# Kernel tuning notes

Hardware: AMD Instinct MI355X
Metric: run time of the kernel (lower is better)

Reference implementation:

```python
import jax, jax.numpy as jnp
import numpy as np

N = 50000
E = 800000


def _degrees(src, dst):
    ones = jnp.ones((E,), dtype=jnp.float32)
    indeg = jax.ops.segment_sum(ones, dst, num_segments=N)
    outdeg = jax.ops.segment_sum(ones, src, num_segments=N)
    return indeg, outdeg


def _aggregate(h, src, dst):
    # update_all(copy_src, sum): gather src features, scatter-add to dst
    return jax.ops.segment_sum(h[src], dst, num_segments=N)


def _graph_conv(h, src, dst, innorm, outnorm, W, b):
    h = h * outnorm[:, None]
    h = _aggregate(h, src, dst)
    h = h * innorm[:, None]
    return h @ W + b


def setup_inputs() -> dict:
    key = jax.random.key(0)
    ks = jax.random.split(key, 8)
    d_in, d_hid, d_out = 128, 128, 64
    inp = {
        "features": jax.random.normal(ks[0], (N, d_in), dtype=jnp.float32),
        "src": jax.random.randint(ks[1], (E,), 0, N, dtype=jnp.int32),
        "dst": jax.random.randint(ks[2], (E,), 0, N, dtype=jnp.int32),
        "W0": jax.random.normal(ks[3], (d_in, d_hid), dtype=jnp.float32) / np.sqrt(d_in),
        "b0": jnp.zeros((d_hid,), dtype=jnp.float32),
        "W1": jax.random.normal(ks[4], (d_hid, d_hid), dtype=jnp.float32) / np.sqrt(d_hid),
        "b1": jnp.zeros((d_hid,), dtype=jnp.float32),
        "W2": jax.random.normal(ks[5], (d_hid, d_hid), dtype=jnp.float32) / np.sqrt(d_hid),
        "b2": jnp.zeros((d_hid,), dtype=jnp.float32),
        "W3": jax.random.normal(ks[6], (d_hid, d_out), dtype=jnp.float32) / np.sqrt(d_hid),
        "b3": jnp.zeros((d_out,), dtype=jnp.float32),
    }
    return inp


def reference(features, src, dst, W0, b0, W1, b1, W2, b2, W3, b3):
    indeg, outdeg = _degrees(src, dst)
    innorm = jnp.power(jnp.clip(indeg, 1.0, None), -0.5)
    outnorm = jnp.power(jnp.clip(outdeg, 1.0, None), -0.5)

    # input GraphConv + relu
    h = jax.nn.relu(_graph_conv(features, src, dst, innorm, outnorm, W0, b0))

    # GResConv blocks: graph_res=True, raw_res=True, dropout=0 (identity)
    for (W, b) in ((W1, b1), (W2, b2)):
        res = features * innorm[:, None]          # pre-norm (in-degree)
        res = _aggregate(res, src, dst)
        res = res * innorm[:, None]               # post-norm (in-degree)
        h = jax.nn.relu(_graph_conv(h, src, dst, innorm, outnorm, W, b) + res)

    # output GraphConv (no activation)
    return _graph_conv(h, src, dst, innorm, outnorm, W3, b3)
```

## Files before the change

kernel.cpp:

```cpp
#include <hip/hip_runtime.h>


#define GN 50000
#define GE 800000
#define SCAN_CHUNK 1024
#define DEG_BLOCKS 64
#define DEG_SLICE 12500
#define HALF_NODES 25000
#define HALF_WORDS 12500

typedef __attribute__((ext_vector_type(8))) short bf16x8;
typedef __attribute__((ext_vector_type(4))) float f32x4;

__device__ __forceinline__ float u2f(unsigned int u) { return __uint_as_float(u); }

__device__ __forceinline__ unsigned int bfr(float a) {
  unsigned int u = __float_as_uint(a);
  return (u + 0x7fffu + ((u >> 16) & 1u)) >> 16;
}
__device__ __forceinline__ unsigned int bfpack(float a, float b) {
  return bfr(a) | (bfr(b) << 16);
}
__device__ __forceinline__ void bfunpack8(uint4 u, float* f) {
  f[0] = u2f(u.x << 16); f[1] = u2f(u.x & 0xffff0000u);
  f[2] = u2f(u.y << 16); f[3] = u2f(u.y & 0xffff0000u);
  f[4] = u2f(u.z << 16); f[5] = u2f(u.z & 0xffff0000u);
  f[6] = u2f(u.w << 16); f[7] = u2f(u.w & 0xffff0000u);
}

__global__ __launch_bounds__(256) void degrees_lds_kernel(
    const int* __restrict__ src, const int* __restrict__ dst,
    unsigned int* __restrict__ partials, int E) {
  __shared__ unsigned int hist[HALF_WORDS];
  for (int i = threadIdx.x; i < HALF_WORDS; i += 256) hist[i] = 0u;
  __syncthreads();
  int b    = blockIdx.x & 63;
  int half = (blockIdx.x >> 6) & 1;
  int dir  = blockIdx.x >> 7;
  const int* __restrict__ idx = dir ? src : dst;
  int lo = half * HALF_NODES, hi = lo + HALF_NODES;
  int s = b * DEG_SLICE;
  int e = min(s + DEG_SLICE, E);
  for (int i = s + threadIdx.x; i < e; i += 256) {
    int node = idx[i];
    if (node >= lo && node < hi) {
      int local = node - lo;
      atomicAdd(&hist[local >> 1], 1u << ((local & 1) << 4));
    }
  }
  __syncthreads();
  unsigned int* outp = partials + (((size_t)dir * 2 + half) * DEG_BLOCKS + b) * HALF_WORDS;
  for (int i = threadIdx.x; i < HALF_WORDS; i += 256) outp[i] = hist[i];
}

__global__ void degrees_reduce_kernel(const unsigned int* __restrict__ partials,
                                      int* __restrict__ indeg, float* __restrict__ innorm,
                                      float* __restrict__ outnorm,
                                      unsigned int* __restrict__ rel16pk) {
  int g = blockIdx.x * blockDim.x + threadIdx.x;
  if (g >= 2 * HALF_WORDS) return;
  int half = (g >= HALF_WORDS) ? 1 : 0;
  int w = g - half * HALF_WORDS;
  int n0 = half * HALF_NODES + 2 * w;
  unsigned int inLo = 0, inHi = 0, outLo = 0, outHi = 0;
  const unsigned int* pIn  = partials + ((size_t)(0 * 2 + half) * DEG_BLOCKS) * HALF_WORDS + w;
  const unsigned int* pOut = partials + ((size_t)(1 * 2 + half) * DEG_BLOCKS) * HALF_WORDS + w;
#pragma unroll 4
  for (int b = 0; b < DEG_BLOCKS; b++) {
    rel16pk[((size_t)b * GN + n0) >> 1] = inLo | (inHi << 16);
    unsigned int v = pIn[(size_t)b * HALF_WORDS];
    inLo += v & 0xffffu; inHi += v >> 16;
    unsigned int u = pOut[(size_t)b * HALF_WORDS];
    outLo += u & 0xffffu; outHi += u >> 16;
  }
  indeg[n0]     = (int)inLo;
  indeg[n0 + 1] = (int)inHi;
  innorm[n0]      = rsqrtf((float)max((int)inLo, 1));
  innorm[n0 + 1]  = rsqrtf((float)max((int)inHi, 1));
  outnorm[n0]     = rsqrtf((float)max((int)outLo, 1));
  outnorm[n0 + 1] = rsqrtf((float)max((int)outHi, 1));
}

__global__ __launch_bounds__(256) void scan_blocksums(const int* __restrict__ deg,
                                                      int* __restrict__ bsums, int n) {
  int tid = threadIdx.x;
  int i = blockIdx.x * SCAN_CHUNK + tid * 4;
  int s = 0;
  if (i + 3 < n) {
    int4 v = *(const int4*)(deg + i);
    s = v.x + v.y + v.z + v.w;
  } else {
    for (int j = 0; j < 4; j++) if (i + j < n) s += deg[i + j];
  }
  for (int off = 32; off; off >>= 1) s += __shfl_down(s, off);
  __shared__ int ws[4];
  if ((tid & 63) == 0) ws[tid >> 6] = s;
  __syncthreads();
  if (tid == 0) bsums[blockIdx.x] = ws[0] + ws[1] + ws[2] + ws[3];
}

__global__ void scan_bsums(const int* __restrict__ bsums, int* __restrict__ bpref,
                           int nb, int* __restrict__ offsets, int n) {
  int tid = threadIdx.x;
  int v = (tid < nb) ? bsums[tid] : 0;
  int incl = v;
  for (int off = 1; off < 64; off <<= 1) {
    int t = __shfl_up(incl, off);
    if (tid >= off) incl += t;
  }
  if (tid < nb) bpref[tid] = incl - v;
  if (tid == 63) offsets[n] = incl;
}

__global__ __launch_bounds__(256) void scan_final(const int* __restrict__ deg,
                                                  const int* __restrict__ bpref,
                                                  int* __restrict__ offsets, int n) {
  int tid = threadIdx.x;
  int i = blockIdx.x * SCAN_CHUNK + tid * 4;
  int v[4];
#pragma unroll
  for (int j = 0; j < 4; j++) v[j] = (i + j < n) ? deg[i + j] : 0;
  int tsum = v[0] + v[1] + v[2] + v[3];
  int incl = tsum;
  for (int off = 1; off < 64; off <<= 1) {
    int t = __shfl_up(incl, off);
    if ((tid & 63) >= off) incl += t;
  }
  __shared__ int wsum[4];
  int wid = tid >> 6, lane = tid & 63;
  if (lane == 63) wsum[wid] = incl;
  __syncthreads();
  int wpref = 0;
  for (int w = 0; w < wid; w++) wpref += wsum[w];
  int run = bpref[blockIdx.x] + wpref + incl - tsum;
#pragma unroll
  for (int j = 0; j < 4; j++) {
    if (i + j < n) offsets[i + j] = run;
    run += v[j];
  }
}

__global__ __launch_bounds__(256) void fill_csr_lds_kernel(
    const int* __restrict__ src, const int* __restrict__ dst,
    const int* __restrict__ offsets, const unsigned short* __restrict__ rel16,
    int* __restrict__ csr, int E) {
  __shared__ unsigned int cnt[HALF_WORDS];
  for (int i = threadIdx.x; i < HALF_WORDS; i += 256) cnt[i] = 0u;
  __syncthreads();
  int b    = blockIdx.x & 63;
  int half = blockIdx.x >> 6;
  int lo = half * HALF_NODES, hi = lo + HALF_NODES;
  int s = b * DEG_SLICE;
  int e = min(s + DEG_SLICE, E);
  const unsigned short* relb = rel16 + (size_t)b * GN;
  for (int i = s + threadIdx.x; i < e; i += 256) {
    int d = dst[i];
    if (d >= lo && d < hi) {
      int local = d - lo;
      int sh = (local & 1) << 4;
      unsigned int old = atomicAdd(&cnt[local >> 1], 1u << sh);
      int rank = (int)((old >> sh) & 0xffffu);
      int pos = offsets[d] + (int)relb[d] + rank;
      csr[pos] = src[i];
    }
  }
}

__global__ __launch_bounds__(256) void f32_to_bf16_kernel(const float* __restrict__ in,
                                                          uint4* __restrict__ out, int n8) {
  int t = blockIdx.x * blockDim.x + threadIdx.x;
  if (t >= n8) return;
  const float4* in4 = (const float4*)in;
  float4 f0 = in4[2 * t], f1 = in4[2 * t + 1];
  uint4 o;
  o.x = bfpack(f0.x, f0.y); o.y = bfpack(f0.z, f0.w);
  o.z = bfpack(f1.x, f1.y); o.w = bfpack(f1.z, f1.w);
  out[t] = o;
}

__global__ __launch_bounds__(256) void wconvert_kernel(
    const float* __restrict__ W0, const float* __restrict__ W1,
    const float* __restrict__ W2, const float* __restrict__ W3,
    unsigned short* __restrict__ wt) {
  int e = blockIdx.x * 256 + threadIdx.x;
  if (e >= 3 * 16384 + 8192) return;
  int m, local, N;
  if (e < 49152) { m = e >> 14; local = e & 16383; N = 128; }
  else { m = 3; local = e - 49152; N = 64; }
  const float* W = (m == 0) ? W0 : (m == 1) ? W1 : (m == 2) ? W2 : W3;
  int k = local / N, n = local % N;
  float v = W[k * N + n];
  unsigned int hi = bfr(v);
  float rem = v - u2f(hi << 16);
  unsigned int lo = bfr(rem);
  size_t hibase = (m < 3) ? (size_t)m * 32768 : 98304;
  size_t lobase = hibase + ((m < 3) ? 16384 : 8192);
  wt[hibase + (size_t)n * 128 + k] = (unsigned short)hi;
  wt[lobase + (size_t)n * 128 + k] = (unsigned short)lo;
}

__global__ __launch_bounds__(256) void aggregate128_bf16_kernel(
    const uint4* __restrict__ hq, const float* __restrict__ gscale,
    const float* __restrict__ wscale, const int* __restrict__ offsets,
    const int* __restrict__ csr, uint4* __restrict__ outq, int n) {
  int node = blockIdx.x * 4 + (threadIdx.x >> 6);
  if (node >= n) return;
  int lane = threadIdx.x & 63;
  int c = lane & 15;
  int p = lane >> 4;
  int s = offsets[node], e = offsets[node + 1];
  float acc[8];
#pragma unroll
  for (int j = 0; j < 8; j++) acc[j] = 0.f;
  int i = s + p;
  for (; i + 4 < e; i += 8) {
    int sn0 = csr[i], sn1 = csr[i + 4];
    uint4 u0 = hq[(size_t)sn0 * 16 + c];
    uint4 u1 = hq[(size_t)sn1 * 16 + c];
    float s0 = gscale[sn0], s1 = gscale[sn1];
    float f0[8], f1[8];
    bfunpack8(u0, f0); bfunpack8(u1, f1);
#pragma unroll
    for (int j = 0; j < 8; j++) acc[j] += f0[j] * s0 + f1[j] * s1;
  }
  if (i < e) {
    int sn = csr[i];
    uint4 u = hq[(size_t)sn * 16 + c];
    float sc = gscale[sn];
    float f[8];
    bfunpack8(u, f);
#pragma unroll
    for (int j = 0; j < 8; j++) acc[j] += f[j] * sc;
  }
#pragma unroll
  for (int off = 32; off >= 16; off >>= 1)
#pragma unroll
    for (int j = 0; j < 8; j++) acc[j] += __shfl_down(acc[j], off);
  if (lane < 16) {
    float w = wscale[node];
    uint4 q;
    q.x = bfpack(acc[0] * w, acc[1] * w); q.y = bfpack(acc[2] * w, acc[3] * w);
    q.z = bfpack(acc[4] * w, acc[5] * w); q.w = bfpack(acc[6] * w, acc[7] * w);
    outq[(size_t)node * 16 + c] = q;
  }
}

__global__ __launch_bounds__(256) void aggregate_dual_bf16_kernel(
    const uint4* __restrict__ hq, const float* __restrict__ g1,
    const float* __restrict__ g2, const float* __restrict__ wscale,
    const int* __restrict__ offsets, const int* __restrict__ csr,
    uint4* __restrict__ out1q, float* __restrict__ out2, int n) {
  int node = blockIdx.x * 4 + (threadIdx.x >> 6);
  if (node >= n) return;
  int lane = threadIdx.x & 63;
  int c = lane & 15;
  int p = lane >> 4;
  int s = offsets[node], e = offsets[node + 1];
  float a1[8], a2[8];
#pragma unroll
  for (int j = 0; j < 8; j++) { a1[j] = 0.f; a2[j] = 0.f; }
  int i = s + p;
  for (; i + 4 < e; i += 8) {
    int sn0 = csr[i], sn1 = csr[i + 4];
    uint4 u0 = hq[(size_t)sn0 * 16 + c];
    uint4 u1 = hq[(size_t)sn1 * 16 + c];
    float g1a = g1[sn0], g2a = g2[sn0];
    float g1b = g1[sn1], g2b = g2[sn1];
    float f0[8], f1[8];
    bfunpack8(u0, f0); bfunpack8(u1, f1);
#pragma unroll
    for (int j = 0; j < 8; j++) {
      a1[j] += f0[j] * g1a + f1[j] * g1b;
      a2[j] += f0[j] * g2a + f1[j] * g2b;
    }
  }
  if (i < e) {
    int sn = csr[i];
    uint4 u = hq[(size_t)sn * 16 + c];
    float g1a = g1[sn], g2a = g2[sn];
    float f[8];
    bfunpack8(u, f);
#pragma unroll
    for (int j = 0; j < 8; j++) { a1[j] += f[j] * g1a; a2[j] += f[j] * g2a; }
  }
#pragma unroll
  for (int off = 32; off >= 16; off >>= 1)
#pragma unroll
    for (int j = 0; j < 8; j++) {
      a1[j] += __shfl_down(a1[j], off);
      a2[j] += __shfl_down(a2[j], off);
    }
  if (lane < 16) {
    float w = wscale[node];
    uint4 q;
    q.x = bfpack(a1[0] * w, a1[1] * w); q.y = bfpack(a1[2] * w, a1[3] * w);
    q.z = bfpack(a1[4] * w, a1[5] * w); q.w = bfpack(a1[6] * w, a1[7] * w);
    out1q[(size_t)node * 16 + c] = q;
    float4* o2 = (float4*)(out2 + (size_t)node * 128);
    o2[2 * c]     = make_float4(a2[0] * w, a2[1] * w, a2[2] * w, a2[3] * w);
    o2[2 * c + 1] = make_float4(a2[4] * w, a2[5] * w, a2[6] * w, a2[7] * w);
  }
}

__global__ __launch_bounds__(256) void aggregate64_bf16_kernel(
    const uint4* __restrict__ hq, const float* __restrict__ gscale,
    const float* __restrict__ wscale, const float* __restrict__ bias,
    const int* __restrict__ offsets, const int* __restrict__ csr,
    float* __restrict__ out, int n) {
  int node = blockIdx.x * 4 + (threadIdx.x >> 6);
  if (node >= n) return;
  int lane = threadIdx.x & 63;
  int c = lane & 7;
  int p = lane >> 3;
  int s = offsets[node], e = offsets[node + 1];
  float acc[8];
#pragma unroll
  for (int j = 0; j < 8; j++) acc[j] = 0.f;
  int i = s + p;
  for (; i + 8 < e; i += 16) {
    int sn0 = csr[i], sn1 = csr[i + 8];
    uint4 u0 = hq[(size_t)sn0 * 8 + c];
    uint4 u1 = hq[(size_t)sn1 * 8 + c];
    float s0 = gscale[sn0], s1 = gscale[sn1];
    float f0[8], f1[8];
    bfunpack8(u0, f0); bfunpack8(u1, f1);
#pragma unroll
    for (int j = 0; j < 8; j++) acc[j] += f0[j] * s0 + f1[j] * s1;
  }
  if (i < e) {
    int sn = csr[i];
    uint4 u = hq[(size_t)sn * 8 + c];
    float sc = gscale[sn];
    float f[8];
    bfunpack8(u, f);
#pragma unroll
    for (int j = 0; j < 8; j++) acc[j] += f[j] * sc;
  }
#pragma unroll
  for (int off = 32; off >= 8; off >>= 1)
#pragma unroll
    for (int j = 0; j < 8; j++) acc[j] += __shfl_down(acc[j], off);
  if (lane < 8) {
    float w = wscale[node];
    const float4* bp = (const float4*)bias;
    float4 b0 = bp[2 * c], b1 = bp[2 * c + 1];
    float4* orow = (float4*)(out + (size_t)node * 64);
    orow[2 * c]     = make_float4(acc[0] * w + b0.x, acc[1] * w + b0.y,
                                  acc[2] * w + b0.z, acc[3] * w + b0.w);
    orow[2 * c + 1] = make_float4(acc[4] * w + b1.x, acc[5] * w + b1.y,
                                  acc[6] * w + b1.z, acc[7] * w + b1.w);
  }
}

template <int NT, bool RELU, bool HAS_BIAS, bool ADD_RES>
__global__ __launch_bounds__(256) void mfma_gemm_kernel(
    const unsigned short* __restrict__ Abf, const unsigned short* __restrict__ Wth,
    const unsigned short* __restrict__ Wtl, const float* __restrict__ bias,
    const float* __restrict__ res, unsigned short* __restrict__ outbf, int M) {
  constexpr int DOUT = NT * 16;
  int wid = threadIdx.x >> 6, lane = threadIdx.x & 63;
  int row0 = (blockIdx.x * 4 + wid) * 32;
  int lr = lane & 15, g = lane >> 4;
  bf16x8 a[2][4];
  bf16x8 zz = {0, 0, 0, 0, 0, 0, 0, 0};
#pragma unroll
  for (int rt = 0; rt < 2; rt++) {
    int r = row0 + rt * 16 + lr;
    if (r < M) {
      const unsigned short* ap = Abf + (size_t)r * 128 + g * 8;
#pragma unroll
      for (int s = 0; s < 4; s++) a[rt][s] = *(const bf16x8*)(ap + s * 32);
    } else {
#pragma unroll
      for (int s = 0; s < 4; s++) a[rt][s] = zz;
    }
  }
#pragma unroll
  for (int ct = 0; ct < NT; ct++) {
    const unsigned short* wph = Wth + (size_t)(ct * 16 + lr) * 128 + g * 8;
    const unsigned short* wpl = Wtl + (size_t)(ct * 16 + lr) * 128 + g * 8;
    bf16x8 wh[4], wl[4];
#pragma unroll
    for (int s = 0; s < 4; s++) {
      wh[s] = *(const bf16x8*)(wph + s * 32);
      wl[s] = *(const bf16x8*)(wpl + s * 32);
    }
    f32x4 acc0 = {0.f, 0.f, 0.f, 0.f}, acc1 = {0.f, 0.f, 0.f, 0.f};
#pragma unroll
    for (int s = 0; s < 4; s++) {
      acc0 = __builtin_amdgcn_mfma_f32_16x16x32_bf16(a[0][s], wh[s], acc0, 0, 0, 0);
      acc0 = __builtin_amdgcn_mfma_f32_16x16x32_bf16(a[0][s], wl[s], acc0, 0, 0, 0);
      acc1 = __builtin_amdgcn_mfma_f32_16x16x32_bf16(a[1][s], wh[s], acc1, 0, 0, 0);
      acc1 = __builtin_amdgcn_mfma_f32_16x16x32_bf16(a[1][s], wl[s], acc1, 0, 0, 0);
    }
    int col = ct * 16 + lr;
    float bv = HAS_BIAS ? bias[col] : 0.f;
#pragma unroll
    for (int rt = 0; rt < 2; rt++) {
      f32x4 acc = rt ? acc1 : acc0;
#pragma unroll
      for (int j = 0; j < 4; j++) {
        int r = row0 + rt * 16 + g * 4 + j;
        if (r < M) {
          float v = acc[j] + bv;
          if (ADD_RES) v += res[(size_t)r * 128 + col];
          if (RELU) v = fmaxf(v, 0.f);
          outbf[(size_t)r * DOUT + col] = (unsigned short)bfr(v);
        }
      }
    }
  }
}

extern "C" void kernel_launch(void* const* d_in, const int* in_sizes, int n_in,
                              void* d_out, int out_size, void* d_ws, size_t ws_size,
                              hipStream_t stream) {
  const float* features = (const float*)d_in[0];
  const int*   src      = (const int*)d_in[1];
  const int*   dst      = (const int*)d_in[2];
  const float* W0 = (const float*)d_in[3];
  const float* b0 = (const float*)d_in[4];
  const float* W1 = (const float*)d_in[5];
  const float* b1 = (const float*)d_in[6];
  const float* W2 = (const float*)d_in[7];
  const float* b2 = (const float*)d_in[8];
  const float* W3 = (const float*)d_in[9];
  const float* b3 = (const float*)d_in[10];
  float* out = (float*)d_out;
  const int N = GN, E = GE;

  char* ws = (char*)d_ws;
  size_t off = 0;
  auto alloc = [&](size_t bytes) -> void* {
    void* p = ws + off;
    off = (off + bytes + 255) & ~(size_t)255;
    return p;
  };
  unsigned int* partials = (unsigned int*)alloc((size_t)2 * 2 * DEG_BLOCKS * HALF_WORDS * 4);
  unsigned int* rel16pk  = (unsigned int*)alloc((size_t)DEG_BLOCKS * GN * 2);
  int*   indeg   = (int*)alloc((size_t)N * 4);
  float* innorm  = (float*)alloc((size_t)N * 4);
  float* outnorm = (float*)alloc((size_t)N * 4);
  int*   offsets = (int*)alloc((size_t)(N + 1) * 4);
  int*   csr     = (int*)alloc((size_t)E * 4);
  int*   bsums   = (int*)alloc((size_t)256 * 4);
  int*   bpref   = (int*)alloc((size_t)256 * 4);
  unsigned short* wt = (unsigned short*)alloc((size_t)114688 * 2);
  uint4* fbf = (uint4*)alloc((size_t)N * 128 * 2);
  float* res = (float*)alloc((size_t)N * 128 * 4);
  unsigned short* tbf = (unsigned short*)alloc((size_t)N * 128 * 2);
  unsigned short* hbf = (unsigned short*)alloc((size_t)N * 128 * 2);
  (void)ws_size; (void)in_sizes; (void)n_in; (void)out_size;

  unsigned short* Ybf = (unsigned short*)res;
  const unsigned short *w0h = wt,          *w0l = wt + 16384;
  const unsigned short *w1h = wt + 32768,  *w1l = wt + 49152;
  const unsigned short *w2h = wt + 65536,  *w2l = wt + 81920;
  const unsigned short *w3h = wt + 98304,  *w3l = wt + 106496;

  degrees_lds_kernel<<<256, 256, 0, stream>>>(src, dst, partials, E);
  degrees_reduce_kernel<<<(2 * HALF_WORDS + 255) / 256, 256, 0, stream>>>(
      partials, indeg, innorm, outnorm, rel16pk);

  int nb = (N + SCAN_CHUNK - 1) / SCAN_CHUNK;
  scan_blocksums<<<nb, 256, 0, stream>>>(indeg, bsums, N);
  scan_bsums<<<1, 64, 0, stream>>>(bsums, bpref, nb, offsets, N);
  scan_final<<<nb, 256, 0, stream>>>(indeg, bpref, offsets, N);

  fill_csr_lds_kernel<<<128, 256, 0, stream>>>(
      src, dst, offsets, (const unsigned short*)rel16pk, csr, E);

  wconvert_kernel<<<(57344 + 255) / 256, 256, 0, stream>>>(W0, W1, W2, W3, wt);
  f32_to_bf16_kernel<<<(N * 128 / 8 + 255) / 256, 256, 0, stream>>>(
      features, fbf, N * 128 / 8);

  int aggGrid  = (N + 3) / 4;
  int gemmGrid = (N + 127) / 128;

  aggregate_dual_bf16_kernel<<<aggGrid, 256, 0, stream>>>(
      fbf, outnorm, innorm, innorm, offsets, csr, (uint4*)tbf, res, N);
  mfma_gemm_kernel<8, true, true, false><<<gemmGrid, 256, 0, stream>>>(
      tbf, w0h, w0l, b0, nullptr, hbf, N);
  aggregate128_bf16_kernel<<<aggGrid, 256, 0, stream>>>(
      (const uint4*)hbf, outnorm, innorm, offsets, csr, (uint4*)tbf, N);
  mfma_gemm_kernel<8, true, true, true><<<gemmGrid, 256, 0, stream>>>(
      tbf, w1h, w1l, b1, res, hbf, N);
  aggregate128_bf16_kernel<<<aggGrid, 256, 0, stream>>>(
      (const uint4*)hbf, outnorm, innorm, offsets, csr, (uint4*)tbf, N);
  mfma_gemm_kernel<8, true, true, true><<<gemmGrid, 256, 0, stream>>>(
      tbf, w2h, w2l, b2, res, hbf, N);
  mfma_gemm_kernel<4, false, false, false><<<gemmGrid, 256, 0, stream>>>(
      hbf, w3h, w3l, nullptr, nullptr, Ybf, N);
  aggregate64_bf16_kernel<<<aggGrid, 256, 0, stream>>>(
      (const uint4*)Ybf, outnorm, innorm, b3, offsets, csr, out, N);
}
```

Measured before the change: 385.3 us.

## Store residual in bf16, pack norms, unroll gathers, widen LDS histogram blocks

Stores the raw residual aggregate in bf16 instead of fp32, halving its write in the dual aggregation and its reads in two GEMM epilogues. Packs out/in norms into a float2 array so the dual aggregation does one gather per neighbor instead of two. Adds a 4-way unrolled gather loop in the 128-wide aggregation kernels to keep more loads in flight, and doubles the block size of the degree and CSR-fill kernels. Rounding the residual to bf16 adds some precision loss.

```diff
diff --git a/kernel.cpp b/kernel.cpp
--- a/kernel.cpp
+++ b/kernel.cpp
@@ -28,11 +28,11 @@
   f[6] = u2f(u.w << 16); f[7] = u2f(u.w & 0xffff0000u);
 }
 
-__global__ __launch_bounds__(256) void degrees_lds_kernel(
+__global__ __launch_bounds__(512) void degrees_lds_kernel(
     const int* __restrict__ src, const int* __restrict__ dst,
     unsigned int* __restrict__ partials, int E) {
   __shared__ unsigned int hist[HALF_WORDS];
-  for (int i = threadIdx.x; i < HALF_WORDS; i += 256) hist[i] = 0u;
+  for (int i = threadIdx.x; i < HALF_WORDS; i += 512) hist[i] = 0u;
   __syncthreads();
   int b    = blockIdx.x & 63;
   int half = (blockIdx.x >> 6) & 1;
@@ -41,7 +41,7 @@
   int lo = half * HALF_NODES, hi = lo + HALF_NODES;
   int s = b * DEG_SLICE;
   int e = min(s + DEG_SLICE, E);
-  for (int i = s + threadIdx.x; i < e; i += 256) {
+  for (int i = s + threadIdx.x; i < e; i += 512) {
     int node = idx[i];
     if (node >= lo && node < hi) {
       int local = node - lo;
@@ -50,12 +50,12 @@
   }
   __syncthreads();
   unsigned int* outp = partials + (((size_t)dir * 2 + half) * DEG_BLOCKS + b) * HALF_WORDS;
-  for (int i = threadIdx.x; i < HALF_WORDS; i += 256) outp[i] = hist[i];
+  for (int i = threadIdx.x; i < HALF_WORDS; i += 512) outp[i] = hist[i];
 }
 
 __global__ void degrees_reduce_kernel(const unsigned int* __restrict__ partials,
                                       int* __restrict__ indeg, float* __restrict__ innorm,
-                                      float* __restrict__ outnorm,
+                                      float* __restrict__ outnorm, float2* __restrict__ nrm2,
                                       unsigned int* __restrict__ rel16pk) {
   int g = blockIdx.x * blockDim.x + threadIdx.x;
   if (g >= 2 * HALF_WORDS) return;
@@ -75,10 +75,12 @@
   }
   indeg[n0]     = (int)inLo;
   indeg[n0 + 1] = (int)inHi;
-  innorm[n0]      = rsqrtf((float)max((int)inLo, 1));
-  innorm[n0 + 1]  = rsqrtf((float)max((int)inHi, 1));
-  outnorm[n0]     = rsqrtf((float)max((int)outLo, 1));
-  outnorm[n0 + 1] = rsqrtf((float)max((int)outHi, 1));
+  float i0 = rsqrtf((float)max((int)inLo, 1)),  i1 = rsqrtf((float)max((int)inHi, 1));
+  float o0 = rsqrtf((float)max((int)outLo, 1)), o1 = rsqrtf((float)max((int)outHi, 1));
+  innorm[n0] = i0; innorm[n0 + 1] = i1;
+  outnorm[n0] = o0; outnorm[n0 + 1] = o1;
+  nrm2[n0]     = make_float2(o0, i0);
+  nrm2[n0 + 1] = make_float2(o1, i1);
 }
 
 __global__ __launch_bounds__(256) void scan_blocksums(const int* __restrict__ deg,
@@ -140,12 +142,12 @@
   }
 }
 
-__global__ __launch_bounds__(256) void fill_csr_lds_kernel(
+__global__ __launch_bounds__(512) void fill_csr_lds_kernel(
     const int* __restrict__ src, const int* __restrict__ dst,
     const int* __restrict__ offsets, const unsigned short* __restrict__ rel16,
     int* __restrict__ csr, int E) {
   __shared__ unsigned int cnt[HALF_WORDS];
-  for (int i = threadIdx.x; i < HALF_WORDS; i += 256) cnt[i] = 0u;
+  for (int i = threadIdx.x; i < HALF_WORDS; i += 512) cnt[i] = 0u;
   __syncthreads();
   int b    = blockIdx.x & 63;
   int half = blockIdx.x >> 6;
@@ -153,7 +155,7 @@
   int s = b * DEG_SLICE;
   int e = min(s + DEG_SLICE, E);
   const unsigned short* relb = rel16 + (size_t)b * GN;
-  for (int i = s + threadIdx.x; i < e; i += 256) {
+  for (int i = s + threadIdx.x; i < e; i += 512) {
     int d = dst[i];
     if (d >= lo && d < hi) {
       int local = d - lo;
@@ -213,6 +215,23 @@
 #pragma unroll
   for (int j = 0; j < 8; j++) acc[j] = 0.f;
   int i = s + p;
+  for (; i + 12 < e; i += 16) {
+    int sn[4];
+#pragma unroll
+    for (int q = 0; q < 4; q++) sn[q] = csr[i + 4 * q];
+    uint4 u[4]; float sv[4];
+#pragma unroll
+    for (int q = 0; q < 4; q++) {
+      u[q] = hq[(size_t)sn[q] * 16 + c];
+      sv[q] = gscale[sn[q]];
+    }
+#pragma unroll
+    for (int q = 0; q < 4; q++) {
+      float f[8]; bfunpack8(u[q], f);
+#pragma unroll
+      for (int j = 0; j < 8; j++) acc[j] += f[j] * sv[q];
+    }
+  }
   for (; i + 4 < e; i += 8) {
     int sn0 = csr[i], sn1 = csr[i + 4];
     uint4 u0 = hq[(size_t)sn0 * 16 + c];
@@ -227,8 +246,7 @@
     int sn = csr[i];
     uint4 u = hq[(size_t)sn * 16 + c];
     float sc = gscale[sn];
-    float f[8];
-    bfunpack8(u, f);
+    float f[8]; bfunpack8(u, f);
 #pragma unroll
     for (int j = 0; j < 8; j++) acc[j] += f[j] * sc;
   }
@@ -246,10 +264,10 @@
 }
 
 __global__ __launch_bounds__(256) void aggregate_dual_bf16_kernel(
-    const uint4* __restrict__ hq, const float* __restrict__ g1,
-    const float* __restrict__ g2, const float* __restrict__ wscale,
-    const int* __restrict__ offsets, const int* __restrict__ csr,
-    uint4* __restrict__ out1q, float* __restrict__ out2, int n) {
+    const uint4* __restrict__ hq, const float2* __restrict__ nrm2,
+    const float* __restrict__ wscale, const int* __restrict__ offsets,
+    const int* __restrict__ csr, uint4* __restrict__ out1q,
+    uint4* __restrict__ out2q, int n) {
   int node = blockIdx.x * 4 + (threadIdx.x >> 6);
   if (node >= n) return;
   int lane = threadIdx.x & 63;
@@ -260,28 +278,46 @@
 #pragma unroll
   for (int j = 0; j < 8; j++) { a1[j] = 0.f; a2[j] = 0.f; }
   int i = s + p;
+  for (; i + 12 < e; i += 16) {
+    int sn[4];
+#pragma unroll
+    for (int q = 0; q < 4; q++) sn[q] = csr[i + 4 * q];
+    uint4 u[4]; float2 g[4];
+#pragma unroll
+    for (int q = 0; q < 4; q++) {
+      u[q] = hq[(size_t)sn[q] * 16 + c];
+      g[q] = nrm2[sn[q]];
+    }
+#pragma unroll
+    for (int q = 0; q < 4; q++) {
+      float f[8]; bfunpack8(u[q], f);
+#pragma unroll
+      for (int j = 0; j < 8; j++) {
+        a1[j] += f[j] * g[q].x;
+        a2[j] += f[j] * g[q].y;
+      }
+    }
+  }
   for (; i + 4 < e; i += 8) {
     int sn0 = csr[i], sn1 = csr[i + 4];
     uint4 u0 = hq[(size_t)sn0 * 16 + c];
     uint4 u1 = hq[(size_t)sn1 * 16 + c];
-    float g1a = g1[sn0], g2a = g2[sn0];
-    float g1b = g1[sn1], g2b = g2[sn1];
+    float2 ga = nrm2[sn0], gb = nrm2[sn1];
     float f0[8], f1[8];
     bfunpack8(u0, f0); bfunpack8(u1, f1);
 #pragma unroll
     for (int j = 0; j < 8; j++) {
-      a1[j] += f0[j] * g1a + f1[j] * g1b;
-      a2[j] += f0[j] * g2a + f1[j] * g2b;
+      a1[j] += f0[j] * ga.x + f1[j] * gb.x;
+      a2[j] += f0[j] * ga.y + f1[j] * gb.y;
     }
   }
   if (i < e) {
     int sn = csr[i];
     uint4 u = hq[(size_t)sn * 16 + c];
-    float g1a = g1[sn], g2a = g2[sn];
-    float f[8];
-    bfunpack8(u, f);
-#pragma unroll
-    for (int j = 0; j < 8; j++) { a1[j] += f[j] * g1a; a2[j] += f[j] * g2a; }
+    float2 ga = nrm2[sn];
+    float f[8]; bfunpack8(u, f);
+#pragma unroll
+    for (int j = 0; j < 8; j++) { a1[j] += f[j] * ga.x; a2[j] += f[j] * ga.y; }
   }
 #pragma unroll
   for (int off = 32; off >= 16; off >>= 1)
@@ -292,13 +328,13 @@
     }
   if (lane < 16) {
     float w = wscale[node];
-    uint4 q;
-    q.x = bfpack(a1[0] * w, a1[1] * w); q.y = bfpack(a1[2] * w, a1[3] * w);
-    q.z = bfpack(a1[4] * w, a1[5] * w); q.w = bfpack(a1[6] * w, a1[7] * w);
-    out1q[(size_t)node * 16 + c] = q;
-    float4* o2 = (float4*)(out2 + (size_t)node * 128);
-    o2[2 * c]     = make_float4(a2[0] * w, a2[1] * w, a2[2] * w, a2[3] * w);
-    o2[2 * c + 1] = make_float4(a2[4] * w, a2[5] * w, a2[6] * w, a2[7] * w);
+    uint4 q1, q2;
+    q1.x = bfpack(a1[0] * w, a1[1] * w); q1.y = bfpack(a1[2] * w, a1[3] * w);
+    q1.z = bfpack(a1[4] * w, a1[5] * w); q1.w = bfpack(a1[6] * w, a1[7] * w);
+    q2.x = bfpack(a2[0] * w, a2[1] * w); q2.y = bfpack(a2[2] * w, a2[3] * w);
+    q2.z = bfpack(a2[4] * w, a2[5] * w); q2.w = bfpack(a2[6] * w, a2[7] * w);
+    out1q[(size_t)node * 16 + c] = q1;
+    out2q[(size_t)node * 16 + c] = q2;
   }
 }
 
@@ -331,8 +367,7 @@
     int sn = csr[i];
     uint4 u = hq[(size_t)sn * 8 + c];
     float sc = gscale[sn];
-    float f[8];
-    bfunpack8(u, f);
+    float f[8]; bfunpack8(u, f);
 #pragma unroll
     for (int j = 0; j < 8; j++) acc[j] += f[j] * sc;
   }
@@ -356,7 +391,7 @@
 __global__ __launch_bounds__(256) void mfma_gemm_kernel(
     const unsigned short* __restrict__ Abf, const unsigned short* __restrict__ Wth,
     const unsigned short* __restrict__ Wtl, const float* __restrict__ bias,
-    const float* __restrict__ res, unsigned short* __restrict__ outbf, int M) {
+    const unsigned short* __restrict__ resbf, unsigned short* __restrict__ outbf, int M) {
   constexpr int DOUT = NT * 16;
   int wid = threadIdx.x >> 6, lane = threadIdx.x & 63;
   int row0 = (blockIdx.x * 4 + wid) * 32;
@@ -403,7 +438,7 @@
         int r = row0 + rt * 16 + g * 4 + j;
         if (r < M) {
           float v = acc[j] + bv;
-          if (ADD_RES) v += res[(size_t)r * 128 + col];
+          if (ADD_RES) v += u2f((unsigned int)resbf[(size_t)r * 128 + col] << 16);
           if (RELU) v = fmaxf(v, 0.f);
           outbf[(size_t)r * DOUT + col] = (unsigned short)bfr(v);
         }
@@ -441,33 +476,34 @@
   int*   indeg   = (int*)alloc((size_t)N * 4);
   float* innorm  = (float*)alloc((size_t)N * 4);
   float* outnorm = (float*)alloc((size_t)N * 4);
+  float2* nrm2   = (float2*)alloc((size_t)N * 8);
   int*   offsets = (int*)alloc((size_t)(N + 1) * 4);
   int*   csr     = (int*)alloc((size_t)E * 4);
   int*   bsums   = (int*)alloc((size_t)256 * 4);
   int*   bpref   = (int*)alloc((size_t)256 * 4);
   unsigned short* wt = (unsigned short*)alloc((size_t)114688 * 2);
   uint4* fbf = (uint4*)alloc((size_t)N * 128 * 2);
-  float* res = (float*)alloc((size_t)N * 128 * 4);
+  unsigned short* resbf = (unsigned short*)alloc((size_t)N * 128 * 2);
   unsigned short* tbf = (unsigned short*)alloc((size_t)N * 128 * 2);
   unsigned short* hbf = (unsigned short*)alloc((size_t)N * 128 * 2);
   (void)ws_size; (void)in_sizes; (void)n_in; (void)out_size;
 
-  unsigned short* Ybf = (unsigned short*)res;
+  unsigned short* Ybf = resbf;
   const unsigned short *w0h = wt,          *w0l = wt + 16384;
   const unsigned short *w1h = wt + 32768,  *w1l = wt + 49152;
   const unsigned short *w2h = wt + 65536,  *w2l = wt + 81920;
   const unsigned short *w3h = wt + 98304,  *w3l = wt + 106496;
 
-  degrees_lds_kernel<<<256, 256, 0, stream>>>(src, dst, partials, E);
+  degrees_lds_kernel<<<256, 512, 0, stream>>>(src, dst, partials, E);
   degrees_reduce_kernel<<<(2 * HALF_WORDS + 255) / 256, 256, 0, stream>>>(
-      partials, indeg, innorm, outnorm, rel16pk);
+      partials, indeg, innorm, outnorm, nrm2, rel16pk);
 
   int nb = (N + SCAN_CHUNK - 1) / SCAN_CHUNK;
   scan_blocksums<<<nb, 256, 0, stream>>>(indeg, bsums, N);
   scan_bsums<<<1, 64, 0, stream>>>(bsums, bpref, nb, offsets, N);
   scan_final<<<nb, 256, 0, stream>>>(indeg, bpref, offsets, N);
 
-  fill_csr_lds_kernel<<<128, 256, 0, stream>>>(
+  fill_csr_lds_kernel<<<128, 512, 0, stream>>>(
       src, dst, offsets, (const unsigned short*)rel16pk, csr, E);
 
   wconvert_kernel<<<(57344 + 255) / 256, 256, 0, stream>>>(W0, W1, W2, W3, wt);
@@ -478,17 +514,17 @@
   int gemmGrid = (N + 127) / 128;
 
   aggregate_dual_bf16_kernel<<<aggGrid, 256, 0, stream>>>(
-      fbf, outnorm, innorm, innorm, offsets, csr, (uint4*)tbf, res, N);
+      fbf, nrm2, innorm, offsets, csr, (uint4*)tbf, (uint4*)resbf, N);
   mfma_gemm_kernel<8, true, true, false><<<gemmGrid, 256, 0, stream>>>(
       tbf, w0h, w0l, b0, nullptr, hbf, N);
   aggregate128_bf16_kernel<<<aggGrid, 256, 0, stream>>>(
       (const uint4*)hbf, outnorm, innorm, offsets, csr, (uint4*)tbf, N);
   mfma_gemm_kernel<8, true, true, true><<<gemmGrid, 256, 0, stream>>>(
-      tbf, w1h, w1l, b1, res, hbf, N);
+      tbf, w1h, w1l, b1, resbf, hbf, N);
   aggregate128_bf16_kernel<<<aggGrid, 256, 0, stream>>>(
       (const uint4*)hbf, outnorm, innorm, offsets, csr, (uint4*)tbf, N);
   mfma_gemm_kernel<8, true, true, true><<<gemmGrid, 256, 0, stream>>>(
-      tbf, w2h, w2l, b2, res, hbf, N);
+      tbf, w2h, w2l, b2, resbf, hbf, N);
   mfma_gemm_kernel<4, false, false, false><<<gemmGrid, 256, 0, stream>>>(
       hbf, w3h, w3l, nullptr, nullptr, Ybf, N);
   aggregate64_bf16_kernel<<<aggGrid, 256, 0, stream>>>(
```

Result: faster. 363.6 us (-5.6%).
